# Kernel tuning notes

Hardware: AMD Instinct MI355X
Metric: run time of the kernel (lower is better)

## Reference

```python
import jax, jax.numpy as jnp
import numpy as np
from jax import lax

B, T, V, E, H = 8, 512, 32000, 256, 512
NEG = -1e9


def setup_inputs() -> dict:
    key = jax.random.key(0)
    ks = jax.random.split(key, 13)
    g = lambda k, shp, sc: (jax.random.normal(k, shp, jnp.float32) * sc)
    return {
        'x': jax.random.randint(ks[0], (B, T), 0, V),
        'lengths': jax.random.randint(ks[1], (B,), T // 2, T + 1),
        'embed': g(ks[2], (V, E), 0.02),
        'W_ih': g(ks[3], (H, E), 1.0 / np.sqrt(E)),
        'W_hh': g(ks[4], (H, H), 1.0 / np.sqrt(H)),
        'b_ih': g(ks[5], (H,), 0.01),
        'b_hh': g(ks[6], (H,), 0.01),
        'attn_W': g(ks[7], (H, 2 * H), 1.0 / np.sqrt(2 * H)),
        'attn_b': g(ks[8], (H,), 0.01),
        'attn_v': g(ks[9], (1, H), 1.0 / np.sqrt(H)),
        'attn_v_b': g(ks[10], (1,), 0.01),
        'fc_W': g(ks[11], (V, 2 * H), 1.0 / np.sqrt(2 * H)),
        'fc_b': g(ks[12], (V,), 0.01),
    }


def reference(x, lengths, embed, W_ih, W_hh, b_ih, b_hh,
              attn_W, attn_b, attn_v, attn_v_b, fc_W, fc_b):
    b, t = x.shape
    h = W_ih.shape[0]
    # embedding with padding_idx=0 (row 0 forced to zero)
    tab = embed.at[0].set(0.0)
    emb = tab[x]  # [B,T,E]
    # vanilla tanh RNN via scan (precompute input projection)
    xin = emb @ W_ih.T + b_ih  # [B,T,H]

    def rnn_step(hprev, xt):
        hnew = jnp.tanh(xt + hprev @ W_hh.T + b_hh)
        return hnew, hnew

    _, out = lax.scan(rnn_step, jnp.zeros((b, h), xin.dtype), xin.transpose(1, 0, 2))
    out = out.transpose(1, 0, 2)  # [B,T,H]
    # pad_packed_sequence zeros hidden states past each sequence length
    len_mask = jnp.arange(t)[None, :] < lengths[:, None]  # [B,T]
    out = out * len_mask[..., None].astype(out.dtype)

    # additive attention: score(t,s) = v . tanh(W1 h_t + W2 h_s + b)
    W1, W2 = attn_W[:, :h], attn_W[:, h:]
    q = out @ W1.T            # [B,T,H]
    k = out @ W2.T + attn_b   # [B,T,H]
    v = attn_v[0]             # [H]

    def att_row(_, qt):  # qt: [B,H] -> scores over all s: [B,T]
        s = jnp.tanh(qt[:, None, :] + k) @ v + attn_v_b[0]
        return None, s

    _, scores = lax.scan(att_row, None, q.transpose(1, 0, 2))  # [T,B,T]
    scores = scores.transpose(1, 0, 2)  # [B,T(query),T(key)]
    causal = jnp.arange(t)[:, None] >= jnp.arange(t)[None, :]  # s <= t
    valid = causal[None] & len_mask[:, None, :]
    scores = jnp.where(valid, scores, NEG)
    alpha = jax.nn.softmax(scores, axis=-1)
    context = jnp.einsum('bts,bsh->bth', alpha, out)  # [B,T,H]
    feats = jnp.concatenate([out, context], axis=-1)  # [B,T,2H]
    logits = feats @ fc_W.T + fc_b  # [B,T,V]
    return logits
```

## Files before the change

kernel.cpp:

```cpp
#include <hip/hip_runtime.h>
#include <hip/hip_bf16.h>

typedef __attribute__((ext_vector_type(8))) short short8;
typedef __attribute__((ext_vector_type(4))) float f32x4;
typedef __attribute__((ext_vector_type(4))) unsigned int u32x4;

__device__ __forceinline__ void glds16(const void* g, void* l) {
  __builtin_amdgcn_global_load_lds(
      (const __attribute__((address_space(1))) unsigned int*)g,
      (__attribute__((address_space(3))) unsigned int*)l, 16, 0, 0);
}

__device__ __forceinline__ void bar_lds() {
  asm volatile("s_waitcnt lgkmcnt(0)\n\ts_barrier" ::: "memory");
}

__device__ __forceinline__ float fast_tanh(float x) {
  float e = __expf(2.0f * x);
  return (e - 1.0f) * __builtin_amdgcn_rcpf(e + 1.0f);
}

__device__ __forceinline__ unsigned short bfh(float f) {
  __hip_bfloat16 h = __float2bfloat16(f);
  return *reinterpret_cast<unsigned short*>(&h);
}
__device__ __forceinline__ float bf2f(unsigned short u) {
  unsigned v = ((unsigned)u) << 16;
  float f;
  __builtin_memcpy(&f, &v, 4);
  return f;
}
__device__ __forceinline__ short bf16r(float f) { return (short)bfh(f); }

union FragU {
  unsigned int u[4];
  short8 s;
};

__global__ __launch_bounds__(256) void k_xin(const int* __restrict__ x, const float* __restrict__ embed,
                                             const float* __restrict__ W_ih, const float* __restrict__ b_ih,
                                             float* __restrict__ xin) {
  __shared__ float At[64][128];
  __shared__ float Bt[128][64];
  const int tid = threadIdx.x;
  const int bt0 = blockIdx.x * 64, j0 = blockIdx.y * 64;
  const int ty = tid >> 4, tx = tid & 15;
  const int lane = tid & 63, cgrp = tid >> 6;
  float acc[4][4] = {};
  for (int kc = 0; kc < 256; kc += 128) {
#pragma unroll
    for (int rr = 0; rr < 8; ++rr) {
      int row = rr * 8 + (tid >> 5);
      int col = (tid & 31) * 4;
      int tok = x[bt0 + row];
      float4 v = make_float4(0.f, 0.f, 0.f, 0.f);
      if (tok != 0) v = *(const float4*)&embed[(size_t)tok * 256 + kc + col];
      *(float4*)&At[row][col] = v;
    }
#pragma unroll
    for (int cc = 0; cc < 8; ++cc) {
      int col = cgrp * 32 + cc * 4;
      float4 v = *(const float4*)&W_ih[(size_t)(j0 + lane) * 256 + kc + col];
      Bt[col + 0][lane] = v.x; Bt[col + 1][lane] = v.y;
      Bt[col + 2][lane] = v.z; Bt[col + 3][lane] = v.w;
    }
    __syncthreads();
    for (int kk = 0; kk < 128; ++kk) {
      float bv[4];
#pragma unroll
      for (int c = 0; c < 4; ++c) bv[c] = Bt[kk][tx * 4 + c];
#pragma unroll
      for (int a = 0; a < 4; ++a) {
        float av = At[ty * 4 + a][kk];
#pragma unroll
        for (int c = 0; c < 4; ++c) acc[a][c] = fmaf(av, bv[c], acc[a][c]);
      }
    }
    __syncthreads();
  }
#pragma unroll
  for (int a = 0; a < 4; ++a) {
    int m = bt0 + ty * 4 + a;
#pragma unroll
    for (int c = 0; c < 4; ++c) {
      int j = j0 + tx * 4 + c;
      xin[(size_t)m * 512 + j] = acc[a][c] + b_ih[j];
    }
  }
}

__global__ __launch_bounds__(512) void k_rnn(const float* __restrict__ xin, const float* __restrict__ W_hh,
                                             const float* __restrict__ b_hh, const int* __restrict__ lengths,
                                             unsigned long long* mbox, float* __restrict__ out,
                                             unsigned short* __restrict__ feats,
                                             const float* __restrict__ fcW, unsigned short* __restrict__ fcWb) {
  const int tid = threadIdx.x;
  if (blockIdx.x >= 8) {
    const size_t stride = (size_t)(gridDim.x - 8) * 512 * 8;
    for (size_t i = ((size_t)(blockIdx.x - 8) * 512 + tid) * 8; i < 32768000ull; i += stride) {
      float4 a = *(const float4*)(fcW + i);
      float4 b = *(const float4*)(fcW + i + 4);
      short8 v;
      v[0] = bf16r(a.x); v[1] = bf16r(a.y); v[2] = bf16r(a.z); v[3] = bf16r(a.w);
      v[4] = bf16r(b.x); v[5] = bf16r(b.y); v[6] = bf16r(b.z); v[7] = bf16r(b.w);
      *(short8*)(fcWb + i) = v;
    }
    return;
  }
  const int blk = blockIdx.x;
  const int w = tid >> 6, l = tid & 63;
  const int jt = w & 3, kh = w >> 2;
  const int j16 = blk * 64 + jt * 16;
  const int r = l & 15;
  const int g = l >> 4;
  const int n = l & 15;

  __shared__ unsigned long long stg[2048];
  __shared__ f32x4 Cbuf[4][64];
  __shared__ float hLf[8][64];
  __shared__ unsigned int hL32[8][64];

  short8 bhi[8], blo[8];
  {
    const float* wrow = &W_hh[(size_t)(j16 + n) * 512];
#pragma unroll
    for (int c8 = 0; c8 < 8; ++c8) {
      int c = kh * 8 + c8;
      const float* wp = wrow + c * 32 + g * 8;
      float4 wa = *(const float4*)wp;
      float4 wb = *(const float4*)(wp + 4);
      float wv[8] = {wa.x, wa.y, wa.z, wa.w, wb.x, wb.y, wb.z, wb.w};
#pragma unroll
      for (int e = 0; e < 8; ++e) {
        unsigned short h = bfh(wv[e]);
        bhi[c8][e] = (short)h;
        blo[c8][e] = (short)bfh(wv[e] - bf2f(h));
      }
    }
  }

  float bj = 0.f, xv[4];
  if (w < 4 && l < 32) {
    bj = b_hh[j16 + n];
#pragma unroll
    for (int i = 0; i < 4; ++i)
      xv[i] = xin[((size_t)(g * 4 + i) * 512 + 0) * 512 + j16 + n];
  }
  const int mylen = lengths[(tid >> 6) & 7];

  __syncthreads();

  const int sgran = tid ^ ((tid >> 6) & 3);

  for (int t = 0; t < 512; ++t) {
    {
      unsigned long long* src = mbox + ((size_t)blk * 16 + (t & 15)) * 2048 + tid * 4;
      u32x4 A, B2;
      int guard = 0;
      while (true) {
        asm volatile(
            "global_load_dwordx4 %0, %2, off sc0 sc1\n\t"
            "global_load_dwordx4 %1, %2, off offset:16 sc0 sc1\n\t"
            "s_waitcnt vmcnt(0)"
            : "=&v"(A), "=&v"(B2)
            : "v"(src)
            : "memory");
        bool ok = true;
#pragma unroll
        for (int q = 0; q < 4; ++q) ok = ok && (A[q] != 0xFFFFFFFFu) && (B2[q] != 0xFFFFFFFFu);
        if (ok || ++guard == (1 << 20)) break;
      }
      stg[sgran * 4 + 0] = (unsigned long long)A[0] | ((unsigned long long)A[1] << 32);
      stg[sgran * 4 + 1] = (unsigned long long)A[2] | ((unsigned long long)A[3] << 32);
      stg[sgran * 4 + 2] = (unsigned long long)B2[0] | ((unsigned long long)B2[1] << 32);
      stg[sgran * 4 + 3] = (unsigned long long)B2[2] | ((unsigned long long)B2[3] << 32);
      u32x4 S;
      S[0] = S[1] = S[2] = S[3] = 0xFFFFFFFFu;
      asm volatile(
          "global_store_dwordx4 %0, %1, off sc0 sc1\n\t"
          "global_store_dwordx4 %0, %1, off offset:16 sc0 sc1"
          :: "v"(src), "v"(S)
          : "memory");
      bar_lds();
    }

    f32x4 acc0 = {}, acc1 = {};
#pragma unroll
    for (int c8 = 0; c8 < 8; ++c8) {
      FragU ah, al;
      if (r < 8) {
        int gran = r * 64 + kh * 32 + c8 * 4 + g;
        int gs = (gran ^ (r & 3)) * 4;
        unsigned long long u0 = stg[gs + 0], u1 = stg[gs + 1];
        unsigned long long u2 = stg[gs + 2], u3 = stg[gs + 3];
        ah.u[0] = (unsigned)u0; al.u[0] = (unsigned)(u0 >> 32);
        ah.u[1] = (unsigned)u1; al.u[1] = (unsigned)(u1 >> 32);
        ah.u[2] = (unsigned)u2; al.u[2] = (unsigned)(u2 >> 32);
        ah.u[3] = (unsigned)u3; al.u[3] = (unsigned)(u3 >> 32);
      } else {
        ah.u[0] = ah.u[1] = ah.u[2] = ah.u[3] = 0u;
        al.u[0] = al.u[1] = al.u[2] = al.u[3] = 0u;
      }
      if (c8 & 1) {
        acc1 = __builtin_amdgcn_mfma_f32_16x16x32_bf16(ah.s, bhi[c8], acc1, 0, 0, 0);
        acc1 = __builtin_amdgcn_mfma_f32_16x16x32_bf16(ah.s, blo[c8], acc1, 0, 0, 0);
        acc1 = __builtin_amdgcn_mfma_f32_16x16x32_bf16(al.s, bhi[c8], acc1, 0, 0, 0);
      } else {
        acc0 = __builtin_amdgcn_mfma_f32_16x16x32_bf16(ah.s, bhi[c8], acc0, 0, 0, 0);
        acc0 = __builtin_amdgcn_mfma_f32_16x16x32_bf16(ah.s, blo[c8], acc0, 0, 0, 0);
        acc0 = __builtin_amdgcn_mfma_f32_16x16x32_bf16(al.s, bhi[c8], acc0, 0, 0, 0);
      }
    }
    f32x4 tot = acc0 + acc1;

    if (w >= 4) Cbuf[w - 4][l] = tot;
    bar_lds();
    if (w < 4) {
      tot += Cbuf[w][l];
      if (l < 32) {
#pragma unroll
        for (int i = 0; i < 4; ++i) {
          int b = g * 4 + i;
          float hn = fast_tanh(xv[i] + tot[i] + bj);
          hLf[b][jt * 16 + n] = hn;
          unsigned hi = bfh(hn);
          unsigned lo = bfh(hn - bf2f((unsigned short)hi));
          hL32[b][jt * 16 + n] = hi | (lo << 16);
        }
        int tt = (t < 511) ? t + 1 : 511;
#pragma unroll
        for (int i = 0; i < 4; ++i)
          xv[i] = xin[((size_t)(g * 4 + i) * 512 + tt) * 512 + j16 + n];
      }
    }
    bar_lds();

    {
      int b = tid >> 6, jl = tid & 63;
      float hv = hLf[b][jl];
      hv = (t < mylen) ? hv : 0.f;
      out[((size_t)b * 512 + t) * 512 + blk * 64 + jl] = hv;
      feats[((size_t)b * 512 + t) * 1024 + blk * 64 + jl] = bfh(hv);
    }

    if (t < 511) {
      unsigned long long* dst = mbox + ((size_t)w * 16 + ((t + 1) & 15)) * 2048 + blk * 32;
      const int e0 = (l & 15) * 4;
#pragma unroll
      for (int k2 = 0; k2 < 2; ++k2) {
        int b = (l >> 4) + k2 * 4;
        unsigned a0 = hL32[b][e0 + 0], a1 = hL32[b][e0 + 1];
        unsigned a2 = hL32[b][e0 + 2], a3 = hL32[b][e0 + 3];
        u32x4 val;
        val[0] = (a0 & 0xffffu) | (a1 << 16);
        val[1] = (a0 >> 16) | (a1 & 0xffff0000u);
        val[2] = (a2 & 0xffffu) | (a3 << 16);
        val[3] = (a2 >> 16) | (a3 & 0xffff0000u);
        unsigned long long* p = dst + (size_t)b * 256 + (l & 15) * 2;
        asm volatile("global_store_dwordx4 %0, %1, off sc0 sc1" :: "v"(p), "v"(val) : "memory");
      }
    }
  }
}

__global__ __launch_bounds__(256) void k_qk(const float* __restrict__ out, const float* __restrict__ attn_W,
                                            const float* __restrict__ attn_b, float* __restrict__ qdst,
                                            float* __restrict__ kdst) {
  __shared__ float At[64][128];
  __shared__ float Bt[128][64];
  const int tid = threadIdx.x;
  const int MODE = blockIdx.z;
  const int bt0 = blockIdx.x * 64, j0 = blockIdx.y * 64;
  const int ty = tid >> 4, tx = tid & 15;
  const int lane = tid & 63, cgrp = tid >> 6;
  float acc[4][4] = {};
  for (int kc = 0; kc < 512; kc += 128) {
#pragma unroll
    for (int rr = 0; rr < 8; ++rr) {
      int row = rr * 8 + (tid >> 5);
      int col = (tid & 31) * 4;
      *(float4*)&At[row][col] = *(const float4*)&out[((size_t)bt0 + row) * 512 + kc + col];
    }
#pragma unroll
    for (int cc = 0; cc < 8; ++cc) {
      int col = cgrp * 32 + cc * 4;
      float4 v = *(const float4*)&attn_W[(size_t)(j0 + lane) * 1024 + (MODE ? 512 : 0) + kc + col];
      Bt[col + 0][lane] = v.x; Bt[col + 1][lane] = v.y;
      Bt[col + 2][lane] = v.z; Bt[col + 3][lane] = v.w;
    }
    __syncthreads();
    for (int kk = 0; kk < 128; ++kk) {
      float bv[4];
#pragma unroll
      for (int c = 0; c < 4; ++c) bv[c] = Bt[kk][tx * 4 + c];
#pragma unroll
      for (int a = 0; a < 4; ++a) {
        float av = At[ty * 4 + a][kk];
#pragma unroll
        for (int c = 0; c < 4; ++c) acc[a][c] = fmaf(av, bv[c], acc[a][c]);
      }
    }
    __syncthreads();
  }
#pragma unroll
  for (int a = 0; a < 4; ++a) {
    int bt = bt0 + ty * 4 + a;
#pragma unroll
    for (int c = 0; c < 4; ++c) {
      int j = j0 + tx * 4 + c;
      if (MODE == 0) {
        qdst[(size_t)bt * 512 + j] = acc[a][c];
      } else {
        int bb = bt >> 9, tt = bt & 511;
        kdst[((size_t)bb * 512 + j) * 512 + tt] = acc[a][c] + attn_b[j];
      }
    }
  }
}

__global__ __launch_bounds__(256) void k_scores(const float* __restrict__ q, const float* __restrict__ kT,
                                                const float* __restrict__ attn_v, const float* __restrict__ attn_v_b,
                                                const int* __restrict__ lengths, float* __restrict__ pbuf,
                                                float* __restrict__ invl) {
  const int b = blockIdx.x, t0 = blockIdx.y * 4;
  const int tid = threadIdx.x;
  __shared__ float qL[4][512];
  __shared__ float vL[512];
  __shared__ float red[4][4];
  for (int i = tid; i < 4 * 512; i += 256) {
    int rr = i >> 9, h = i & 511;
    qL[rr][h] = q[((size_t)b * 512 + t0 + rr) * 512 + h];
  }
  for (int i = tid; i < 512; i += 256) vL[i] = attn_v[i];
  const float vb = attn_v_b[0];
  const int len = lengths[b];
  __syncthreads();
  const int s_hi = min(t0 + 3, len - 1);
  const float* kTb = kT + (size_t)b * 512 * 512;
  float psum[4] = {0.f, 0.f, 0.f, 0.f};
#pragma unroll
  for (int si = 0; si < 2; ++si) {
    int s = tid + si * 256;
    float acc[4] = {0.f, 0.f, 0.f, 0.f};
    if (s <= s_hi) {
      for (int h = 0; h < 512; ++h) {
        float kv = kTb[(size_t)h * 512 + s];
        float vh = vL[h];
#pragma unroll
        for (int rr = 0; rr < 4; ++rr) acc[rr] = fmaf(vh, fast_tanh(qL[rr][h] + kv), acc[rr]);
      }
    }
#pragma unroll
    for (int rr = 0; rr < 4; ++rr) {
      int t = t0 + rr;
      bool valid = (s <= t) && (s < len);
      float p = valid ? __expf(acc[rr] + vb - 20.f) : 0.f;
      pbuf[((size_t)b * 512 + t) * 512 + s] = p;
      psum[rr] += p;
    }
  }
  const int wv = tid >> 6, ln = tid & 63;
#pragma unroll
  for (int rr = 0; rr < 4; ++rr) {
    float v = psum[rr];
#pragma unroll
    for (int m = 1; m < 64; m <<= 1) v += __shfl_xor(v, m);
    if (ln == 0) red[wv][rr] = v;
  }
  __syncthreads();
  if (tid < 4) {
    float s = red[0][tid] + red[1][tid] + red[2][tid] + red[3][tid];
    invl[(size_t)b * 512 + t0 + tid] = 1.0f / s;
  }
}

__global__ __launch_bounds__(256) void k_context(const float* __restrict__ pbuf, const float* __restrict__ out,
                                                 const float* __restrict__ invl, unsigned short* __restrict__ feats) {
  __shared__ float Pt[64][128];
  __shared__ float Ot[128][64];
  const int b = blockIdx.z, t0 = blockIdx.y * 64, h0 = blockIdx.x * 64;
  const int tid = threadIdx.x, ty = tid >> 4, tx = tid & 15;
  float acc[4][4] = {};
  for (int sc = 0; sc < 512; sc += 128) {
#pragma unroll
    for (int rr = 0; rr < 8; ++rr) {
      int row = rr * 8 + (tid >> 5);
      int col = (tid & 31) * 4;
      *(float4*)&Pt[row][col] = *(const float4*)&pbuf[((size_t)b * 512 + t0 + row) * 512 + sc + col];
    }
#pragma unroll
    for (int rr = 0; rr < 8; ++rr) {
      int srow = rr * 16 + (tid >> 4);
      int col = (tid & 15) * 4;
      *(float4*)&Ot[srow][col] = *(const float4*)&out[((size_t)b * 512 + sc + srow) * 512 + h0 + col];
    }
    __syncthreads();
    for (int kk = 0; kk < 128; ++kk) {
      float ov[4];
#pragma unroll
      for (int c = 0; c < 4; ++c) ov[c] = Ot[kk][tx * 4 + c];
#pragma unroll
      for (int a = 0; a < 4; ++a) {
        float pv = Pt[ty * 4 + a][kk];
#pragma unroll
        for (int c = 0; c < 4; ++c) acc[a][c] = fmaf(pv, ov[c], acc[a][c]);
      }
    }
    __syncthreads();
  }
#pragma unroll
  for (int a = 0; a < 4; ++a) {
    int t = t0 + ty * 4 + a;
    float il = invl[b * 512 + t];
#pragma unroll
    for (int c = 0; c < 4; ++c) {
      int h = h0 + tx * 4 + c;
      feats[((size_t)b * 512 + t) * 1024 + 512 + h] = (unsigned short)bf16r(acc[a][c] * il);
    }
  }
}

__global__ __launch_bounds__(256) void k_logits(const unsigned short* __restrict__ A,
                                                const unsigned short* __restrict__ Bw,
                                                const float* __restrict__ bias, float* __restrict__ C) {
  const int linb = blockIdx.x;
  const int xcd = linb & 7, pos = linb >> 3;
  const int m0 = (xcd * 4 + (pos & 3)) * 128;
  const int n0 = (pos >> 2) * 128;
  __shared__ unsigned short As[128 * 64];
  __shared__ unsigned short Bs[128 * 64];
  const int tid = threadIdx.x;
  const int wave = tid >> 6, lane = tid & 63;
  const int wm = (wave >> 1) * 64, wn = (wave & 1) * 64;
  const int lo16 = lane & 15, oct = lane >> 4;
  f32x4 acc[4][4] = {};
  for (int kt = 0; kt < 1024; kt += 64) {
#pragma unroll
    for (int i = 0; i < 4; ++i) {
      int ci = wave * 4 + i;
      int mrow = ci * 8 + (lane >> 3);
      int k8 = (lane & 7) * 8;
      glds16(&A[(size_t)(m0 + mrow) * 1024 + kt + k8], &As[ci * 512]);
      glds16(&Bw[(size_t)(n0 + mrow) * 1024 + kt + k8], &Bs[ci * 512]);
    }
    __syncthreads();
#pragma unroll
    for (int kk = 0; kk < 2; ++kk) {
      short8 af[4], bf[4];
#pragma unroll
      for (int i = 0; i < 4; ++i)
        af[i] = *(const short8*)&As[(wm + i * 16 + lo16) * 64 + kk * 32 + oct * 8];
#pragma unroll
      for (int jn = 0; jn < 4; ++jn)
        bf[jn] = *(const short8*)&Bs[(wn + jn * 16 + lo16) * 64 + kk * 32 + oct * 8];
#pragma unroll
      for (int i = 0; i < 4; ++i)
#pragma unroll
        for (int jn = 0; jn < 4; ++jn)
          acc[i][jn] = __builtin_amdgcn_mfma_f32_16x16x32_bf16(af[i], bf[jn], acc[i][jn], 0, 0, 0);
    }
    __syncthreads();
  }
#pragma unroll
  for (int jn = 0; jn < 4; ++jn) {
    int nn = n0 + wn + jn * 16 + lo16;
    float bv = bias[nn];
#pragma unroll
    for (int i = 0; i < 4; ++i) {
      int mbase = m0 + wm + i * 16 + oct * 4;
#pragma unroll
      for (int rr = 0; rr < 4; ++rr)
        C[(size_t)(mbase + rr) * 32000 + nn] = acc[i][jn][rr] + bv;
    }
  }
}

extern "C" void kernel_launch(void* const* d_in, const int* in_sizes, int n_in,
                              void* d_out, int out_size, void* d_ws, size_t ws_size,
                              hipStream_t stream) {
  const int* x = (const int*)d_in[0];
  const int* lengths = (const int*)d_in[1];
  const float* embed = (const float*)d_in[2];
  const float* W_ih = (const float*)d_in[3];
  const float* W_hh = (const float*)d_in[4];
  const float* b_ih = (const float*)d_in[5];
  const float* b_hh = (const float*)d_in[6];
  const float* attn_W = (const float*)d_in[7];
  const float* attn_b = (const float*)d_in[8];
  const float* attn_v = (const float*)d_in[9];
  const float* attn_v_b = (const float*)d_in[10];
  const float* fc_W = (const float*)d_in[11];
  const float* fc_b = (const float*)d_in[12];
  float* logits = (float*)d_out;

  char* ws = (char*)d_ws;
  const size_t MB8 = 8388608;
  float* xin  = (float*)(ws);
  float* outp = (float*)(ws + 1 * MB8);
  float* q    = (float*)(ws + 2 * MB8);
  float* kT   = (float*)(ws + 3 * MB8);
  float* pbuf = (float*)(ws + 4 * MB8);
  float* invl = (float*)(ws + 5 * MB8);
  unsigned short* feats = (unsigned short*)(ws + 5 * MB8 + 16384);
  unsigned short* fcWb  = (unsigned short*)(ws + 6 * MB8 + 16384);
  unsigned long long* mbox = (unsigned long long*)pbuf;

  hipMemsetAsync(mbox, 0xFF, 8 * 16 * 16384, stream);
  for (int d = 0; d < 8; ++d)
    hipMemsetAsync((char*)mbox + (size_t)d * 16 * 16384, 0x00, 16384, stream);
  k_xin<<<dim3(64, 8), 256, 0, stream>>>(x, embed, W_ih, b_ih, xin);
  k_rnn<<<136, 512, 0, stream>>>(xin, W_hh, b_hh, lengths, mbox, outp, feats, fc_W, fcWb);
  k_qk<<<dim3(64, 8, 2), 256, 0, stream>>>(outp, attn_W, attn_b, q, kT);
  k_scores<<<dim3(8, 128), 256, 0, stream>>>(q, kT, attn_v, attn_v_b, lengths, pbuf, invl);
  k_context<<<dim3(8, 8, 8), 256, 0, stream>>>(pbuf, outp, invl, feats);
  k_logits<<<8000, 256, 0, stream>>>(feats, fcWb, fc_b, logits);
}
```

Before: 2.250 ms.

## Fuse attention scores and context into one kernel; defer mailbox reset in RNN

The score kernel and the context GEMM are merged. Softmax probabilities now stay in LDS and each block computes the context rows for its own 4 queries, with the loop stopping at the causal and length bound. This removes the pbuf round trip and one launch. In the RNN loop, the mailbox slot reset and the output/feats stores are moved after the next-step publish, taking them off the critical path between steps. The fused context loop re-reads `out` for every 4-query block and uses scalar FMAs, so it gives up the reuse of the tiled GEMM.

New measurement: 2.381 ms. 1.06x slower.

```diff
diff --git a/kernel.cpp b/kernel.cpp
--- a/kernel.cpp
+++ b/kernel.cpp
@@ -153,8 +153,8 @@
   const int sgran = tid ^ ((tid >> 6) & 3);
 
   for (int t = 0; t < 512; ++t) {
+    unsigned long long* slotp = mbox + ((size_t)blk * 16 + (t & 15)) * 2048 + tid * 4;
     {
-      unsigned long long* src = mbox + ((size_t)blk * 16 + (t & 15)) * 2048 + tid * 4;
       u32x4 A, B2;
       int guard = 0;
       while (true) {
@@ -163,7 +163,7 @@
             "global_load_dwordx4 %1, %2, off offset:16 sc0 sc1\n\t"
             "s_waitcnt vmcnt(0)"
             : "=&v"(A), "=&v"(B2)
-            : "v"(src)
+            : "v"(slotp)
             : "memory");
         bool ok = true;
 #pragma unroll
@@ -174,13 +174,6 @@
       stg[sgran * 4 + 1] = (unsigned long long)A[2] | ((unsigned long long)A[3] << 32);
       stg[sgran * 4 + 2] = (unsigned long long)B2[0] | ((unsigned long long)B2[1] << 32);
       stg[sgran * 4 + 3] = (unsigned long long)B2[2] | ((unsigned long long)B2[3] << 32);
-      u32x4 S;
-      S[0] = S[1] = S[2] = S[3] = 0xFFFFFFFFu;
-      asm volatile(
-          "global_store_dwordx4 %0, %1, off sc0 sc1\n\t"
-          "global_store_dwordx4 %0, %1, off offset:16 sc0 sc1"
-          :: "v"(src), "v"(S)
-          : "memory");
       bar_lds();
     }
 
@@ -235,14 +228,6 @@
     }
     bar_lds();
 
-    {
-      int b = tid >> 6, jl = tid & 63;
-      float hv = hLf[b][jl];
-      hv = (t < mylen) ? hv : 0.f;
-      out[((size_t)b * 512 + t) * 512 + blk * 64 + jl] = hv;
-      feats[((size_t)b * 512 + t) * 1024 + blk * 64 + jl] = bfh(hv);
-    }
-
     if (t < 511) {
       unsigned long long* dst = mbox + ((size_t)w * 16 + ((t + 1) & 15)) * 2048 + blk * 32;
       const int e0 = (l & 15) * 4;
@@ -259,6 +244,20 @@
         unsigned long long* p = dst + (size_t)b * 256 + (l & 15) * 2;
         asm volatile("global_store_dwordx4 %0, %1, off sc0 sc1" :: "v"(p), "v"(val) : "memory");
       }
+      u32x4 S;
+      S[0] = S[1] = S[2] = S[3] = 0xFFFFFFFFu;
+      asm volatile(
+          "global_store_dwordx4 %0, %1, off sc0 sc1\n\t"
+          "global_store_dwordx4 %0, %1, off offset:16 sc0 sc1"
+          :: "v"(slotp), "v"(S)
+          : "memory");
+    }
+    {
+      int b = tid >> 6, jl = tid & 63;
+      float hv = hLf[b][jl];
+      hv = (t < mylen) ? hv : 0.f;
+      out[((size_t)b * 512 + t) * 512 + blk * 64 + jl] = hv;
+      feats[((size_t)b * 512 + t) * 1024 + blk * 64 + jl] = bfh(hv);
     }
   }
 }
@@ -318,15 +317,18 @@
   }
 }
 
-__global__ __launch_bounds__(256) void k_scores(const float* __restrict__ q, const float* __restrict__ kT,
-                                                const float* __restrict__ attn_v, const float* __restrict__ attn_v_b,
-                                                const int* __restrict__ lengths, float* __restrict__ pbuf,
-                                                float* __restrict__ invl) {
+__global__ __launch_bounds__(256) void k_attn(const float* __restrict__ q, const float* __restrict__ kT,
+                                              const float* __restrict__ attn_v, const float* __restrict__ attn_v_b,
+                                              const int* __restrict__ lengths, const float* __restrict__ out,
+                                              unsigned short* __restrict__ feats) {
   const int b = blockIdx.x, t0 = blockIdx.y * 4;
   const int tid = threadIdx.x;
   __shared__ float qL[4][512];
   __shared__ float vL[512];
+  __shared__ float pL[4][512];
   __shared__ float red[4][4];
+  __shared__ float inv4[4];
+  __shared__ float tile[64][128];
   for (int i = tid; i < 4 * 512; i += 256) {
     int rr = i >> 9, h = i & 511;
     qL[rr][h] = q[((size_t)b * 512 + t0 + rr) * 512 + h];
@@ -355,68 +357,46 @@
       int t = t0 + rr;
       bool valid = (s <= t) && (s < len);
       float p = valid ? __expf(acc[rr] + vb - 20.f) : 0.f;
-      pbuf[((size_t)b * 512 + t) * 512 + s] = p;
+      pL[rr][s] = p;
       psum[rr] += p;
     }
   }
-  const int wv = tid >> 6, ln = tid & 63;
-#pragma unroll
-  for (int rr = 0; rr < 4; ++rr) {
-    float v = psum[rr];
-#pragma unroll
-    for (int m = 1; m < 64; m <<= 1) v += __shfl_xor(v, m);
-    if (ln == 0) red[wv][rr] = v;
+  {
+    const int wv = tid >> 6, ln = tid & 63;
+#pragma unroll
+    for (int rr = 0; rr < 4; ++rr) {
+      float v = psum[rr];
+#pragma unroll
+      for (int m = 1; m < 64; m <<= 1) v += __shfl_xor(v, m);
+      if (ln == 0) red[wv][rr] = v;
+    }
   }
   __syncthreads();
-  if (tid < 4) {
-    float s = red[0][tid] + red[1][tid] + red[2][tid] + red[3][tid];
-    invl[(size_t)b * 512 + t0 + tid] = 1.0f / s;
-  }
-}
-
-__global__ __launch_bounds__(256) void k_context(const float* __restrict__ pbuf, const float* __restrict__ out,
-                                                 const float* __restrict__ invl, unsigned short* __restrict__ feats) {
-  __shared__ float Pt[64][128];
-  __shared__ float Ot[128][64];
-  const int b = blockIdx.z, t0 = blockIdx.y * 64, h0 = blockIdx.x * 64;
-  const int tid = threadIdx.x, ty = tid >> 4, tx = tid & 15;
-  float acc[4][4] = {};
-  for (int sc = 0; sc < 512; sc += 128) {
-#pragma unroll
-    for (int rr = 0; rr < 8; ++rr) {
-      int row = rr * 8 + (tid >> 5);
-      int col = (tid & 31) * 4;
-      *(float4*)&Pt[row][col] = *(const float4*)&pbuf[((size_t)b * 512 + t0 + row) * 512 + sc + col];
-    }
-#pragma unroll
-    for (int rr = 0; rr < 8; ++rr) {
-      int srow = rr * 16 + (tid >> 4);
-      int col = (tid & 15) * 4;
-      *(float4*)&Ot[srow][col] = *(const float4*)&out[((size_t)b * 512 + sc + srow) * 512 + h0 + col];
-    }
-    __syncthreads();
-    for (int kk = 0; kk < 128; ++kk) {
-      float ov[4];
-#pragma unroll
-      for (int c = 0; c < 4; ++c) ov[c] = Ot[kk][tx * 4 + c];
-#pragma unroll
-      for (int a = 0; a < 4; ++a) {
-        float pv = Pt[ty * 4 + a][kk];
-#pragma unroll
-        for (int c = 0; c < 4; ++c) acc[a][c] = fmaf(pv, ov[c], acc[a][c]);
-      }
-    }
-    __syncthreads();
-  }
-#pragma unroll
-  for (int a = 0; a < 4; ++a) {
-    int t = t0 + ty * 4 + a;
-    float il = invl[b * 512 + t];
-#pragma unroll
-    for (int c = 0; c < 4; ++c) {
-      int h = h0 + tx * 4 + c;
-      feats[((size_t)b * 512 + t) * 1024 + 512 + h] = (unsigned short)bf16r(acc[a][c] * il);
-    }
+  if (tid < 4) inv4[tid] = 1.0f / (red[0][tid] + red[1][tid] + red[2][tid] + red[3][tid]);
+  __syncthreads();
+
+  const int hpos = tid & 127;
+  const int r0 = (tid >> 7) * 2;
+  for (int hc = 0; hc < 4; ++hc) {
+    float a0 = 0.f, a1 = 0.f;
+    for (int s0 = 0; s0 <= s_hi; s0 += 64) {
+#pragma unroll
+      for (int it = 0; it < 8; ++it) {
+        int ss = it * 8 + (tid >> 5);
+        int c4 = (tid & 31) * 4;
+        *(float4*)&tile[ss][c4] = *(const float4*)&out[((size_t)b * 512 + s0 + ss) * 512 + hc * 128 + c4];
+      }
+      __syncthreads();
+      int sl = min(64, s_hi - s0 + 1);
+      for (int ss = 0; ss < sl; ++ss) {
+        float ov = tile[ss][hpos];
+        a0 = fmaf(pL[r0][s0 + ss], ov, a0);
+        a1 = fmaf(pL[r0 + 1][s0 + ss], ov, a1);
+      }
+      __syncthreads();
+    }
+    feats[((size_t)b * 512 + t0 + r0) * 1024 + 512 + hc * 128 + hpos] = bfh(a0 * inv4[r0]);
+    feats[((size_t)b * 512 + t0 + r0 + 1) * 1024 + 512 + hc * 128 + hpos] = bfh(a1 * inv4[r0 + 1]);
   }
 }
 
@@ -500,7 +480,6 @@
   float* q    = (float*)(ws + 2 * MB8);
   float* kT   = (float*)(ws + 3 * MB8);
   float* pbuf = (float*)(ws + 4 * MB8);
-  float* invl = (float*)(ws + 5 * MB8);
   unsigned short* feats = (unsigned short*)(ws + 5 * MB8 + 16384);
   unsigned short* fcWb  = (unsigned short*)(ws + 6 * MB8 + 16384);
   unsigned long long* mbox = (unsigned long long*)pbuf;
@@ -511,7 +490,6 @@
   k_xin<<<dim3(64, 8), 256, 0, stream>>>(x, embed, W_ih, b_ih, xin);
   k_rnn<<<136, 512, 0, stream>>>(xin, W_hh, b_hh, lengths, mbox, outp, feats, fc_W, fcWb);
   k_qk<<<dim3(64, 8, 2), 256, 0, stream>>>(outp, attn_W, attn_b, q, kT);
-  k_scores<<<dim3(8, 128), 256, 0, stream>>>(q, kT, attn_v, attn_v_b, lengths, pbuf, invl);
-  k_context<<<dim3(8, 8, 8), 256, 0, stream>>>(pbuf, outp, invl, feats);
+  k_attn<<<dim3(8, 128), 256, 0, stream>>>(q, kT, attn_v, attn_v_b, lengths, outp, feats);
   k_logits<<<8000, 256, 0, stream>>>(feats, fcWb, fc_b, logits);
 }
```
